# Kernel tuning notes

Hardware: AMD Instinct MI355X
Metric: run time of the kernel (lower is better)

## Reference

```python
import jax, jax.numpy as jnp
import numpy as np

DIM = 768
HEADS = 12
HEAD_DIM = DIM // HEADS
SCALE = DIM ** (-0.5)  # NOTE: module scales by full dim, not head_dim


def setup_inputs() -> dict:
    key = jax.random.key(0)
    k1, k2, k3 = jax.random.split(key, 3)
    B, N = 4, 2048
    x = jax.random.normal(k1, (B, N, DIM), dtype=jnp.float32)
    W_qkv = jax.random.normal(k2, (DIM, 3 * DIM), dtype=jnp.float32) * (DIM ** -0.5)
    W_proj = jax.random.normal(k3, (DIM, DIM), dtype=jnp.float32) * (DIM ** -0.5)
    b_proj = jnp.zeros((DIM,), dtype=jnp.float32)
    return {"x": x, "W_qkv": W_qkv, "W_proj": W_proj, "b_proj": b_proj}


def reference(x, W_qkv, W_proj, b_proj):
    B, N, C = x.shape
    qkv = x @ W_qkv  # [B, N, 3C]
    qkv = qkv.reshape(B, N, 3, HEADS, HEAD_DIM)
    qkv = jnp.transpose(qkv, (2, 0, 3, 1, 4))  # [3, B, H, N, hd]
    q, k, v = qkv[0], qkv[1], qkv[2]
    att = jnp.einsum('bhnd,bhmd->bhnm', q, k) * SCALE
    att = jax.nn.softmax(att, axis=-1)
    # drop=0.0 -> dropout is identity
    out = jnp.einsum('bhnm,bhmd->bhnd', att, v)  # [B, H, N, hd]
    out = jnp.transpose(out, (0, 2, 1, 3)).reshape(B, N, C)
    return out @ W_proj + b_proj
```

## Files before the change

### kernel.cpp

```cpp
#include <hip/hip_runtime.h>
#include <hip/hip_bf16.h>

#define HEADS 12
#define HD    64
#define SEQ   2048
#define CDIM  768
#define QKV_SCALE 0.03608439182435161f
#define LOG2E 1.4426950408889634f
#define SM_C (QKV_SCALE * LOG2E)

typedef __attribute__((ext_vector_type(8))) short bf16x8;
typedef __attribute__((ext_vector_type(4))) float f32x4;
typedef __attribute__((ext_vector_type(4))) unsigned short usx4;
typedef __attribute__((ext_vector_type(8))) unsigned short usx8;
typedef __attribute__((ext_vector_type(2))) unsigned int uix2;
typedef __attribute__((ext_vector_type(4))) unsigned int uix4;

__device__ __forceinline__ unsigned short f2bf(float f) {
  union { __hip_bfloat16 h; unsigned short u; } c;
  c.h = __float2bfloat16(f);
  return c.u;
}

__device__ __forceinline__ float exp2_fast(float x) {
  float r; asm("v_exp_f32 %0, %1" : "=v"(r) : "v"(x)); return r;
}

__device__ __forceinline__ unsigned int cvt_pk_bf16(float lo, float hi) {
  unsigned int r; asm("v_cvt_pk_bf16_f32 %0, %1, %2" : "=v"(r) : "v"(lo), "v"(hi)); return r;
}

__device__ __forceinline__ void gload_lds16(const unsigned short* g, unsigned short* l) {
  __builtin_amdgcn_global_load_lds(
      (__attribute__((address_space(1))) void*)(g),
      (__attribute__((address_space(3))) void*)(l), 16, 0, 0);
}

__global__ __launch_bounds__(256) void k_prep(
    const float* __restrict__ x, unsigned short* __restrict__ xb,
    const float* __restrict__ Wqkv, unsigned short* __restrict__ WqkvT,
    const float* __restrict__ Wproj, unsigned short* __restrict__ WprojT) {
  __shared__ float tile[32][33];
  const int b = blockIdx.x;
  if (b < 3072) {
    int i = b * 256 + threadIdx.x;
    const float4* s4 = (const float4*)x;
    float4 a = s4[i * 2 + 0];
    float4 d = s4[i * 2 + 1];
    usx8 r;
    r[0] = f2bf(a.x); r[1] = f2bf(a.y); r[2] = f2bf(a.z); r[3] = f2bf(a.w);
    r[4] = f2bf(d.x); r[5] = f2bf(d.y); r[6] = f2bf(d.z); r[7] = f2bf(d.w);
    *(usx8*)&xb[i * 8] = r;
    return;
  }
  const float* src; unsigned short* dst; int C, c0, k0;
  if (b < 4800) {
    int tb = b - 3072;
    src = Wqkv; dst = WqkvT; C = 2304;
    c0 = (tb % 72) * 32; k0 = (tb / 72) * 32;
  } else {
    int tb = b - 4800;
    src = Wproj; dst = WprojT; C = 768;
    c0 = (tb % 24) * 32; k0 = (tb / 24) * 32;
  }
  int tx = threadIdx.x & 31;
  int ty = threadIdx.x >> 5;
#pragma unroll
  for (int i = 0; i < 32; i += 8)
    tile[ty + i][tx] = src[(size_t)(k0 + ty + i) * C + c0 + tx];
  __syncthreads();
#pragma unroll
  for (int i = 0; i < 32; i += 8)
    dst[(size_t)(c0 + ty + i) * 768 + k0 + tx] = f2bf(tile[tx][ty + i]);
}

__global__ __launch_bounds__(256, 4) void k_qkv_gemm(
    const unsigned short* __restrict__ A,
    const unsigned short* __restrict__ Bt,
    unsigned short* __restrict__ Qb, unsigned short* __restrict__ Kb,
    unsigned short* __restrict__ Vt) {
  __shared__ unsigned short As[4][128 * 32];
  __shared__ unsigned short Bs[4][128 * 32];
  const int lane = threadIdx.x & 63, w = threadIdx.x >> 6;
  const int g = lane >> 4, c = lane & 15;
  const int wm = w >> 1, wn = w & 1;
  const int id = blockIdx.y * 18 + blockIdx.x;
  const int lin = (id & 7) * 144 + (id >> 3);
  const int r0 = (lin / 18) * 128, c0 = (lin % 18) * 128;
  f32x4 acc[4][4] = {};

  const unsigned short* aptr[2];
  const unsigned short* bptr[2];
#pragma unroll
  for (int i = 0; i < 2; ++i) {
    int e = (w * 2 + i) * 512 + lane * 8;
    int row = e >> 5;
    int cc = ((e >> 3) & 3) ^ ((row >> 1) & 3);
    aptr[i] = A  + (size_t)(r0 + row) * 768 + cc * 8;
    bptr[i] = Bt + (size_t)(c0 + row) * 768 + cc * 8;
  }

  const int sg = g ^ ((c >> 1) & 3);
  int offA[4], offB[4];
#pragma unroll
  for (int f = 0; f < 4; ++f) {
    offA[f] = (wm * 64 + f * 16 + c) * 32 + sg * 8;
    offB[f] = (wn * 64 + f * 16 + c) * 32 + sg * 8;
  }

  auto STAGE = [&](int k0, int b) {
#pragma unroll
    for (int i = 0; i < 2; ++i) {
      gload_lds16(aptr[i] + k0, &As[b][(w * 2 + i) * 512]);
      gload_lds16(bptr[i] + k0, &Bs[b][(w * 2 + i) * 512]);
    }
  };

  STAGE(0, 0);
  STAGE(32, 1);
  asm volatile("s_waitcnt vmcnt(4)" ::: "memory");
  __syncthreads();

#pragma unroll
  for (int t = 0; t < 24; ++t) {
    if (t + 2 < 24) {
      STAGE((t + 2) * 32, (t + 2) & 3);
      asm volatile("s_waitcnt vmcnt(8)" ::: "memory");
    } else if (t + 2 == 24) {
      asm volatile("s_waitcnt vmcnt(4)" ::: "memory");
    } else {
      asm volatile("s_waitcnt vmcnt(0)" ::: "memory");
    }
    __syncthreads();

    const int buf = t & 3;
    bf16x8 af[4], bfr[4];
#pragma unroll
    for (int f = 0; f < 4; ++f) {
      af[f]  = *(const bf16x8*)&As[buf][offA[f]];
      bfr[f] = *(const bf16x8*)&Bs[buf][offB[f]];
    }
    __builtin_amdgcn_s_setprio(1);
#pragma unroll
    for (int fm = 0; fm < 4; ++fm)
#pragma unroll
      for (int fn = 0; fn < 4; ++fn)
        acc[fm][fn] = __builtin_amdgcn_mfma_f32_16x16x32_bf16(af[fm], bfr[fn], acc[fm][fn], 0, 0, 0);
    __builtin_amdgcn_s_setprio(0);
  }

  const int which = c0 / 768;
  const float qsc = (which == 0) ? SM_C : 1.0f;
#pragma unroll
  for (int fm = 0; fm < 4; ++fm) {
    int gr0 = r0 + wm * 64 + fm * 16 + ((lane >> 4) << 2);
    int bb = gr0 >> 11, n0 = gr0 & 2047;
#pragma unroll
    for (int fn = 0; fn < 4; ++fn) {
      int gc = c0 + wn * 64 + fn * 16 + (lane & 15);
      int rem = gc - which * 768;
      int h = rem >> 6, d = rem & 63;
      int bh = bb * HEADS + h;
      f32x4 v = acc[fm][fn];
      if (which == 2) {
        usx4 p;
        p[0] = f2bf(v[0]); p[1] = f2bf(v[1]); p[2] = f2bf(v[2]); p[3] = f2bf(v[3]);
        *(usx4*)&Vt[(size_t)(bh * 64 + d) * 2048 + n0] = p;
      } else {
        unsigned short* dst = (which == 0 ? Qb : Kb) + (size_t)(bh * 2048 + n0) * 64 + d;
        dst[0]   = f2bf(v[0] * qsc);
        dst[64]  = f2bf(v[1] * qsc);
        dst[128] = f2bf(v[2] * qsc);
        dst[192] = f2bf(v[3] * qsc);
      }
    }
  }
}

__global__ __launch_bounds__(256, 2) void k_attn(
    const unsigned short* __restrict__ Qb, const unsigned short* __restrict__ Kb,
    const unsigned short* __restrict__ Vt, unsigned short* __restrict__ Ob) {
  __shared__ unsigned short Ksm[2][64 * 64];
  __shared__ unsigned short Vsm[2][64 * 64];
  const int lane = threadIdx.x & 63, w = threadIdx.x >> 6;
  const int g = lane >> 4, c = lane & 15;

  int id = blockIdx.x + (blockIdx.y << 4);
  int lin = (id & 7) * 96 + (id >> 3);
  int bx = lin & 15, bh = lin >> 4;
  const int q0 = bx * 128 + w * 32;
  const int bb = bh / HEADS, h = bh % HEADS;

  const unsigned short* Qp = Qb + (size_t)bh * SEQ * HD;
  const unsigned short* Kp = Kb + (size_t)bh * SEQ * HD;
  const unsigned short* Vp = Vt + (size_t)bh * HD * SEQ;

  bf16x8 aQ[2][2];
#pragma unroll
  for (int qf = 0; qf < 2; ++qf)
#pragma unroll
    for (int ks = 0; ks < 2; ++ks)
      aQ[qf][ks] = *(const bf16x8*)&Qp[(size_t)(q0 + qf * 16 + c) * 64 + ks * 32 + g * 8];

  float lrun[2] = {0.f, 0.f};
  f32x4 accOT[4][2] = {};
  const f32x4 fzero = {0.f, 0.f, 0.f, 0.f};

  int offf[2][4];
#pragma unroll
  for (int ks = 0; ks < 2; ++ks)
#pragma unroll
    for (int f = 0; f < 4; ++f) {
      int row = f * 16 + c;
      offf[ks][f] = row * 64 + (((ks * 4 + g) ^ (row & 7)) * 8);
    }

  const int eo0 = (w * 2 + 0) * 512 + lane * 8;
  const int row0 = eo0 >> 6, cc0 = ((eo0 >> 3) & 7) ^ (row0 & 7);
  const int eo1 = (w * 2 + 1) * 512 + lane * 8;
  const int row1 = eo1 >> 6, cc1 = ((eo1 >> 3) & 7) ^ (row1 & 7);
  const unsigned short* kga = Kp + (size_t)row0 * 64 + cc0 * 8;
  const unsigned short* kgb = Kp + (size_t)row1 * 64 + cc1 * 8;
  const unsigned short* vga = Vp + (size_t)row0 * 2048 + cc0 * 8;
  const unsigned short* vgb = Vp + (size_t)row1 * 2048 + cc1 * 8;

  gload_lds16(kga, &Ksm[0][(w * 2 + 0) * 512]);
  gload_lds16(kgb, &Ksm[0][(w * 2 + 1) * 512]);
  gload_lds16(vga, &Vsm[0][(w * 2 + 0) * 512]);
  gload_lds16(vgb, &Vsm[0][(w * 2 + 1) * 512]);
  asm volatile("s_waitcnt vmcnt(0)" ::: "memory");
  __syncthreads();

  auto TILE = [&](int t, int buf) {
    if (t + 1 < 32) {
      gload_lds16(kga + (t + 1) * 4096, &Ksm[buf ^ 1][(w * 2 + 0) * 512]);
      gload_lds16(kgb + (t + 1) * 4096, &Ksm[buf ^ 1][(w * 2 + 1) * 512]);
      gload_lds16(vga + (t + 1) * 64,   &Vsm[buf ^ 1][(w * 2 + 0) * 512]);
      gload_lds16(vgb + (t + 1) * 64,   &Vsm[buf ^ 1][(w * 2 + 1) * 512]);
    }

    bf16x8 kf0[4], kf1[4];
#pragma unroll
    for (int fm = 0; fm < 4; ++fm) {
      kf0[fm] = *(const bf16x8*)&Ksm[buf][offf[0][fm]];
      kf1[fm] = *(const bf16x8*)&Ksm[buf][offf[1][fm]];
    }
    f32x4 st[4][2];
    __builtin_amdgcn_s_setprio(1);
#pragma unroll
    for (int fm = 0; fm < 4; ++fm)
#pragma unroll
      for (int qf = 0; qf < 2; ++qf)
        st[fm][qf] = __builtin_amdgcn_mfma_f32_16x16x32_bf16(kf0[fm], aQ[qf][0], fzero, 0, 0, 0);
#pragma unroll
    for (int fm = 0; fm < 4; ++fm)
#pragma unroll
      for (int qf = 0; qf < 2; ++qf)
        st[fm][qf] = __builtin_amdgcn_mfma_f32_16x16x32_bf16(kf1[fm], aQ[qf][1], st[fm][qf], 0, 0, 0);
    __builtin_amdgcn_s_setprio(0);

    uix4 pfrag[2][2];
#pragma unroll
    for (int qf = 0; qf < 2; ++qf) {
      float p[4][4];
      float ts[4];
#pragma unroll
      for (int fm = 0; fm < 4; ++fm) {
        p[fm][0] = exp2_fast(st[fm][qf][0]);
        p[fm][1] = exp2_fast(st[fm][qf][1]);
        p[fm][2] = exp2_fast(st[fm][qf][2]);
        p[fm][3] = exp2_fast(st[fm][qf][3]);
        ts[fm] = (p[fm][0] + p[fm][1]) + (p[fm][2] + p[fm][3]);
      }
      lrun[qf] += (ts[0] + ts[1]) + (ts[2] + ts[3]);

#pragma unroll
      for (int ks = 0; ks < 2; ++ks)
#pragma unroll
        for (int tt = 0; tt < 2; ++tt) {
          unsigned int a = cvt_pk_bf16(p[2 * ks][2 * tt], p[2 * ks][2 * tt + 1]);
          unsigned int b = cvt_pk_bf16(p[2 * ks + 1][2 * tt], p[2 * ks + 1][2 * tt + 1]);
          uix2 s1 = __builtin_amdgcn_permlane32_swap(a, b, false, false);
          uix2 s2 = __builtin_amdgcn_permlane16_swap(s1[0], s1[1], false, false);
          pfrag[ks][qf][tt] = s2[0];
          pfrag[ks][qf][2 + tt] = s2[1];
        }
    }

    bf16x8 vf0[4], vf1[4];
#pragma unroll
    for (int fd = 0; fd < 4; ++fd) {
      vf0[fd] = *(const bf16x8*)&Vsm[buf][offf[0][fd]];
      vf1[fd] = *(const bf16x8*)&Vsm[buf][offf[1][fd]];
    }
    __builtin_amdgcn_s_setprio(1);
#pragma unroll
    for (int fd = 0; fd < 4; ++fd)
#pragma unroll
      for (int qf = 0; qf < 2; ++qf) {
        accOT[fd][qf] = __builtin_amdgcn_mfma_f32_16x16x32_bf16(
            vf0[fd], *(const bf16x8*)&pfrag[0][qf], accOT[fd][qf], 0, 0, 0);
        accOT[fd][qf] = __builtin_amdgcn_mfma_f32_16x16x32_bf16(
            vf1[fd], *(const bf16x8*)&pfrag[1][qf], accOT[fd][qf], 0, 0, 0);
      }
    __builtin_amdgcn_s_setprio(0);

    asm volatile("s_waitcnt vmcnt(0)" ::: "memory");
    __syncthreads();
  };

  for (int kt = 0; kt < 32; kt += 2) {
    TILE(kt, 0);
    TILE(kt + 1, 1);
  }

#pragma unroll
  for (int qf = 0; qf < 2; ++qf) {
    float l = lrun[qf];
    l += __shfl_xor(l, 16);
    l += __shfl_xor(l, 32);
    float rl = 1.0f / l;
    int n = q0 + qf * 16 + c;
#pragma unroll
    for (int fd = 0; fd < 4; ++fd) {
      f32x4 v = accOT[fd][qf];
      usx4 pk;
      pk[0] = f2bf(v[0] * rl); pk[1] = f2bf(v[1] * rl);
      pk[2] = f2bf(v[2] * rl); pk[3] = f2bf(v[3] * rl);
      *(usx4*)&Ob[(size_t)(bb * SEQ + n) * CDIM + h * HD + fd * 16 + 4 * g] = pk;
    }
  }
}

__global__ __launch_bounds__(256) void k_proj_gemm(
    const unsigned short* __restrict__ A,
    const unsigned short* __restrict__ Bt,
    const float* __restrict__ bias, float* __restrict__ out) {
  __shared__ unsigned short As[2][64 * 64];
  __shared__ unsigned short Bs[2][128 * 64];
  const int lane = threadIdx.x & 63, w = threadIdx.x >> 6;
  const int wm = w & 1, wn = w >> 1;
  const int id = blockIdx.y * 6 + blockIdx.x;
  const int lin = (id & 7) * 96 + (id >> 3);
  const int r0 = (lin / 6) * 64, c0 = (lin % 6) * 128;
  f32x4 acc[2][4] = {};

  const unsigned short* aptr[2];
  const unsigned short* bptr[4];
#pragma unroll
  for (int iss = 0; iss < 2; ++iss) {
    int e = (w * 2 + iss) * 512 + lane * 8;
    int row = e >> 6, cc = ((e >> 3) & 7) ^ (row & 7);
    aptr[iss] = A + (size_t)(r0 + row) * 768 + cc * 8;
  }
#pragma unroll
  for (int iss = 0; iss < 4; ++iss) {
    int e = (w * 4 + iss) * 512 + lane * 8;
    int row = e >> 6, cc = ((e >> 3) & 7) ^ (row & 7);
    bptr[iss] = Bt + (size_t)(c0 + row) * 768 + cc * 8;
  }

  auto STAGE = [&](int k0, int b) {
#pragma unroll
    for (int iss = 0; iss < 2; ++iss)
      gload_lds16(aptr[iss] + k0, &As[b][(w * 2 + iss) * 512]);
#pragma unroll
    for (int iss = 0; iss < 4; ++iss)
      gload_lds16(bptr[iss] + k0, &Bs[b][(w * 4 + iss) * 512]);
  };

  STAGE(0, 0);
  asm volatile("s_waitcnt vmcnt(0)" ::: "memory");
  __syncthreads();

  auto KSTEP = [&](int t, int buf) {
    if (t + 1 < 12) STAGE((t + 1) * 64, buf ^ 1);
#pragma unroll
    for (int ks = 0; ks < 2; ++ks) {
      bf16x8 af[2], bfr[4];
#pragma unroll
      for (int f = 0; f < 2; ++f) {
        int ar = wm * 32 + f * 16 + (lane & 15);
        int ac = (ks * 4 + (lane >> 4)) ^ (ar & 7);
        af[f] = *(const bf16x8*)&As[buf][ar * 64 + ac * 8];
      }
#pragma unroll
      for (int f = 0; f < 4; ++f) {
        int br = wn * 64 + f * 16 + (lane & 15);
        int bc = (ks * 4 + (lane >> 4)) ^ (br & 7);
        bfr[f] = *(const bf16x8*)&Bs[buf][br * 64 + bc * 8];
      }
#pragma unroll
      for (int fm = 0; fm < 2; ++fm)
#pragma unroll
        for (int fn = 0; fn < 4; ++fn)
          acc[fm][fn] = __builtin_amdgcn_mfma_f32_16x16x32_bf16(af[fm], bfr[fn], acc[fm][fn], 0, 0, 0);
    }
    asm volatile("s_waitcnt vmcnt(0)" ::: "memory");
    __syncthreads();
  };

  for (int t = 0; t < 12; t += 2) {
    KSTEP(t, 0);
    KSTEP(t + 1, 1);
  }

#pragma unroll
  for (int fm = 0; fm < 2; ++fm) {
    int gr0 = r0 + wm * 32 + fm * 16 + ((lane >> 4) << 2);
#pragma unroll
    for (int fn = 0; fn < 4; ++fn) {
      int gc = c0 + wn * 64 + fn * 16 + (lane & 15);
      float bsv = bias[gc];
      f32x4 v = acc[fm][fn];
#pragma unroll
      for (int r = 0; r < 4; ++r)
        out[(size_t)(gr0 + r) * CDIM + gc] = v[r] + bsv;
    }
  }
}

extern "C" void kernel_launch(void* const* d_in, const int* in_sizes, int n_in,
                              void* d_out, int out_size, void* d_ws, size_t ws_size,
                              hipStream_t stream) {
  const float* x      = (const float*)d_in[0];
  const float* W_qkv  = (const float*)d_in[1];
  const float* W_proj = (const float*)d_in[2];
  const float* b_proj = (const float*)d_in[3];
  float* out = (float*)d_out;

  unsigned short* ws     = (unsigned short*)d_ws;
  unsigned short* xb     = ws;
  unsigned short* WqkvT  = xb + 6291456;
  unsigned short* WprojT = WqkvT + 1769472;
  unsigned short* Qb     = WprojT + 589824;
  unsigned short* Kb     = Qb + 6291456;
  unsigned short* Vt     = Kb + 6291456;
  unsigned short* Ob     = Vt + 6291456;

  k_prep<<<5376, 256, 0, stream>>>(x, xb, W_qkv, WqkvT, W_proj, WprojT);
  k_qkv_gemm<<<dim3(18, 64), 256, 0, stream>>>(xb, WqkvT, Qb, Kb, Vt);
  k_attn<<<dim3(16, 48), 256, 0, stream>>>(Qb, Kb, Vt, Ob);
  k_proj_gemm<<<dim3(6, 128), 256, 0, stream>>>(Ob, WprojT, b_proj, out);
}
```

Baseline: 137.4 us.

## Use 4-buffer K/V ring with prefetch distance two and single barrier in attention

The attention kernel moves from double-buffered K/V LDS tiles with a full vmcnt(0) drain plus barrier at the end of each tile to a 4-slot ring. Loads run two tiles ahead, with partial vmcnt waits and one barrier per tile. The GEMM and attention kernels also replace __syncthreads with raw s_barrier, which skips the LDS waitcnt the compiler normally inserts. The aim is to hide global-load latency and cut barrier stalls, but LDS use doubles to 64KB per block, which may limit the 2 blocks/CU occupancy. Dropping the end-of-tile barrier also relies on the 4-deep ring to avoid overwriting a buffer other waves are still reading.

```diff
diff --git a/kernel.cpp b/kernel.cpp
--- a/kernel.cpp
+++ b/kernel.cpp
@@ -119,7 +119,7 @@
   STAGE(0, 0);
   STAGE(32, 1);
   asm volatile("s_waitcnt vmcnt(4)" ::: "memory");
-  __syncthreads();
+  __builtin_amdgcn_s_barrier();
 
 #pragma unroll
   for (int t = 0; t < 24; ++t) {
@@ -131,7 +131,7 @@
     } else {
       asm volatile("s_waitcnt vmcnt(0)" ::: "memory");
     }
-    __syncthreads();
+    __builtin_amdgcn_s_barrier();
 
     const int buf = t & 3;
     bf16x8 af[4], bfr[4];
@@ -180,8 +180,8 @@
 __global__ __launch_bounds__(256, 2) void k_attn(
     const unsigned short* __restrict__ Qb, const unsigned short* __restrict__ Kb,
     const unsigned short* __restrict__ Vt, unsigned short* __restrict__ Ob) {
-  __shared__ unsigned short Ksm[2][64 * 64];
-  __shared__ unsigned short Vsm[2][64 * 64];
+  __shared__ unsigned short Ksm[4][64 * 64];
+  __shared__ unsigned short Vsm[4][64 * 64];
   const int lane = threadIdx.x & 63, w = threadIdx.x >> 6;
   const int g = lane >> 4, c = lane & 15;
 
@@ -224,20 +224,28 @@
   const unsigned short* vga = Vp + (size_t)row0 * 2048 + cc0 * 8;
   const unsigned short* vgb = Vp + (size_t)row1 * 2048 + cc1 * 8;
 
-  gload_lds16(kga, &Ksm[0][(w * 2 + 0) * 512]);
-  gload_lds16(kgb, &Ksm[0][(w * 2 + 1) * 512]);
-  gload_lds16(vga, &Vsm[0][(w * 2 + 0) * 512]);
-  gload_lds16(vgb, &Vsm[0][(w * 2 + 1) * 512]);
-  asm volatile("s_waitcnt vmcnt(0)" ::: "memory");
-  __syncthreads();
+  auto STAGE = [&](int t, int b) {
+    gload_lds16(kga + t * 4096, &Ksm[b][(w * 2 + 0) * 512]);
+    gload_lds16(kgb + t * 4096, &Ksm[b][(w * 2 + 1) * 512]);
+    gload_lds16(vga + t * 64,   &Vsm[b][(w * 2 + 0) * 512]);
+    gload_lds16(vgb + t * 64,   &Vsm[b][(w * 2 + 1) * 512]);
+  };
+
+  STAGE(0, 0);
+  STAGE(1, 1);
+  asm volatile("s_waitcnt vmcnt(4)" ::: "memory");
+  __builtin_amdgcn_s_barrier();
 
   auto TILE = [&](int t, int buf) {
-    if (t + 1 < 32) {
-      gload_lds16(kga + (t + 1) * 4096, &Ksm[buf ^ 1][(w * 2 + 0) * 512]);
-      gload_lds16(kgb + (t + 1) * 4096, &Ksm[buf ^ 1][(w * 2 + 1) * 512]);
-      gload_lds16(vga + (t + 1) * 64,   &Vsm[buf ^ 1][(w * 2 + 0) * 512]);
-      gload_lds16(vgb + (t + 1) * 64,   &Vsm[buf ^ 1][(w * 2 + 1) * 512]);
-    }
+    if (t + 2 < 32) {
+      STAGE(t + 2, (t + 2) & 3);
+      asm volatile("s_waitcnt vmcnt(8)" ::: "memory");
+    } else if (t + 2 == 32) {
+      asm volatile("s_waitcnt vmcnt(4)" ::: "memory");
+    } else {
+      asm volatile("s_waitcnt vmcnt(0)" ::: "memory");
+    }
+    __builtin_amdgcn_s_barrier();
 
     bf16x8 kf0[4], kf1[4];
 #pragma unroll
@@ -304,14 +312,13 @@
             vf1[fd], *(const bf16x8*)&pfrag[1][qf], accOT[fd][qf], 0, 0, 0);
       }
     __builtin_amdgcn_s_setprio(0);
-
-    asm volatile("s_waitcnt vmcnt(0)" ::: "memory");
-    __syncthreads();
   };
 
-  for (int kt = 0; kt < 32; kt += 2) {
+  for (int kt = 0; kt < 32; kt += 4) {
     TILE(kt, 0);
     TILE(kt + 1, 1);
+    TILE(kt + 2, 2);
+    TILE(kt + 3, 3);
   }
 
 #pragma unroll
```

New measurement: 142.2 us. 3.5% more time.

## Pipeline projection GEMM with 4-stage BK=32 ring and raw barriers

Applied to the files above, without the earlier changes.

The output projection GEMM moves from a 2-buffer BK=64 double-buffer to a 4-slot BK=32 ring with two stages in flight, using counted vmcnt waits instead of draining all loads each step. Fragment offsets are precomputed with a new XOR swizzle, and the MFMA block is raised to higher priority. The QKV GEMM and the new loop use s_barrier in place of __syncthreads, and launch bounds request 3 blocks per CU. The aim is better overlap of global-to-LDS loads with MFMA work and less barrier overhead, at the cost of more loop iterations and reliance on correct hand-counted waitcnts.

```diff
diff --git a/kernel.cpp b/kernel.cpp
--- a/kernel.cpp
+++ b/kernel.cpp
@@ -119,7 +119,7 @@
   STAGE(0, 0);
   STAGE(32, 1);
   asm volatile("s_waitcnt vmcnt(4)" ::: "memory");
-  __syncthreads();
+  __builtin_amdgcn_s_barrier();
 
 #pragma unroll
   for (int t = 0; t < 24; ++t) {
@@ -131,7 +131,7 @@
     } else {
       asm volatile("s_waitcnt vmcnt(0)" ::: "memory");
     }
-    __syncthreads();
+    __builtin_amdgcn_s_barrier();
 
     const int buf = t & 3;
     bf16x8 af[4], bfr[4];
@@ -332,77 +332,80 @@
   }
 }
 
-__global__ __launch_bounds__(256) void k_proj_gemm(
+__global__ __launch_bounds__(256, 3) void k_proj_gemm(
     const unsigned short* __restrict__ A,
     const unsigned short* __restrict__ Bt,
     const float* __restrict__ bias, float* __restrict__ out) {
-  __shared__ unsigned short As[2][64 * 64];
-  __shared__ unsigned short Bs[2][128 * 64];
+  __shared__ unsigned short As[4][64 * 32];
+  __shared__ unsigned short Bs[4][128 * 32];
   const int lane = threadIdx.x & 63, w = threadIdx.x >> 6;
+  const int g = lane >> 4, c = lane & 15;
   const int wm = w & 1, wn = w >> 1;
   const int id = blockIdx.y * 6 + blockIdx.x;
   const int lin = (id & 7) * 96 + (id >> 3);
   const int r0 = (lin / 6) * 64, c0 = (lin % 6) * 128;
   f32x4 acc[2][4] = {};
 
-  const unsigned short* aptr[2];
-  const unsigned short* bptr[4];
-#pragma unroll
-  for (int iss = 0; iss < 2; ++iss) {
-    int e = (w * 2 + iss) * 512 + lane * 8;
-    int row = e >> 6, cc = ((e >> 3) & 7) ^ (row & 7);
-    aptr[iss] = A + (size_t)(r0 + row) * 768 + cc * 8;
-  }
-#pragma unroll
-  for (int iss = 0; iss < 4; ++iss) {
-    int e = (w * 4 + iss) * 512 + lane * 8;
-    int row = e >> 6, cc = ((e >> 3) & 7) ^ (row & 7);
-    bptr[iss] = Bt + (size_t)(c0 + row) * 768 + cc * 8;
-  }
+  const unsigned short* aptr;
+  {
+    int e = w * 512 + lane * 8;
+    int row = e >> 5;
+    int cc = ((e >> 3) & 3) ^ ((row >> 1) & 3);
+    aptr = A + (size_t)(r0 + row) * 768 + cc * 8;
+  }
+  const unsigned short* bptr[2];
+#pragma unroll
+  for (int i = 0; i < 2; ++i) {
+    int e = (w * 2 + i) * 512 + lane * 8;
+    int row = e >> 5;
+    int cc = ((e >> 3) & 3) ^ ((row >> 1) & 3);
+    bptr[i] = Bt + (size_t)(c0 + row) * 768 + cc * 8;
+  }
+
+  const int sg = g ^ ((c >> 1) & 3);
+  int offA[2], offB[4];
+#pragma unroll
+  for (int f = 0; f < 2; ++f) offA[f] = (wm * 32 + f * 16 + c) * 32 + sg * 8;
+#pragma unroll
+  for (int f = 0; f < 4; ++f) offB[f] = (wn * 64 + f * 16 + c) * 32 + sg * 8;
 
   auto STAGE = [&](int k0, int b) {
-#pragma unroll
-    for (int iss = 0; iss < 2; ++iss)
-      gload_lds16(aptr[iss] + k0, &As[b][(w * 2 + iss) * 512]);
-#pragma unroll
-    for (int iss = 0; iss < 4; ++iss)
-      gload_lds16(bptr[iss] + k0, &Bs[b][(w * 4 + iss) * 512]);
+    gload_lds16(aptr + k0, &As[b][w * 512]);
+#pragma unroll
+    for (int i = 0; i < 2; ++i)
+      gload_lds16(bptr[i] + k0, &Bs[b][(w * 2 + i) * 512]);
   };
 
   STAGE(0, 0);
-  asm volatile("s_waitcnt vmcnt(0)" ::: "memory");
-  __syncthreads();
-
-  auto KSTEP = [&](int t, int buf) {
-    if (t + 1 < 12) STAGE((t + 1) * 64, buf ^ 1);
-#pragma unroll
-    for (int ks = 0; ks < 2; ++ks) {
-      bf16x8 af[2], bfr[4];
-#pragma unroll
-      for (int f = 0; f < 2; ++f) {
-        int ar = wm * 32 + f * 16 + (lane & 15);
-        int ac = (ks * 4 + (lane >> 4)) ^ (ar & 7);
-        af[f] = *(const bf16x8*)&As[buf][ar * 64 + ac * 8];
-      }
-#pragma unroll
-      for (int f = 0; f < 4; ++f) {
-        int br = wn * 64 + f * 16 + (lane & 15);
-        int bc = (ks * 4 + (lane >> 4)) ^ (br & 7);
-        bfr[f] = *(const bf16x8*)&Bs[buf][br * 64 + bc * 8];
-      }
-#pragma unroll
-      for (int fm = 0; fm < 2; ++fm)
-#pragma unroll
-        for (int fn = 0; fn < 4; ++fn)
-          acc[fm][fn] = __builtin_amdgcn_mfma_f32_16x16x32_bf16(af[fm], bfr[fn], acc[fm][fn], 0, 0, 0);
-    }
-    asm volatile("s_waitcnt vmcnt(0)" ::: "memory");
-    __syncthreads();
-  };
-
-  for (int t = 0; t < 12; t += 2) {
-    KSTEP(t, 0);
-    KSTEP(t + 1, 1);
+  STAGE(32, 1);
+  asm volatile("s_waitcnt vmcnt(3)" ::: "memory");
+  __builtin_amdgcn_s_barrier();
+
+#pragma unroll
+  for (int t = 0; t < 24; ++t) {
+    if (t + 2 < 24) {
+      STAGE((t + 2) * 32, (t + 2) & 3);
+      asm volatile("s_waitcnt vmcnt(6)" ::: "memory");
+    } else if (t + 2 == 24) {
+      asm volatile("s_waitcnt vmcnt(3)" ::: "memory");
+    } else {
+      asm volatile("s_waitcnt vmcnt(0)" ::: "memory");
+    }
+    __builtin_amdgcn_s_barrier();
+
+    const int buf = t & 3;
+    bf16x8 af[2], bfr[4];
+#pragma unroll
+    for (int f = 0; f < 2; ++f) af[f] = *(const bf16x8*)&As[buf][offA[f]];
+#pragma unroll
+    for (int f = 0; f < 4; ++f) bfr[f] = *(const bf16x8*)&Bs[buf][offB[f]];
+    __builtin_amdgcn_s_setprio(1);
+#pragma unroll
+    for (int fm = 0; fm < 2; ++fm)
+#pragma unroll
+      for (int fn = 0; fn < 4; ++fn)
+        acc[fm][fn] = __builtin_amdgcn_mfma_f32_16x16x32_bf16(af[fm], bfr[fn], acc[fm][fn], 0, 0, 0);
+    __builtin_amdgcn_s_setprio(0);
   }
 
 #pragma unroll
```

Result: no change. 140.0 us (+1.9%).
